# Kernel optimization log

Hardware: AMD Instinct MI355X
Metric: run time of the kernel (lower is better)

The kernel has to match this reference:

```python
import jax, jax.numpy as jnp
import numpy as np

VOCAB = 21
EPS = 1e-5


def rmsnorm(x, w):
    return x * jax.lax.rsqrt(jnp.mean(x * x, axis=-1, keepdims=True) + EPS) * w


def mamba_layer(h, in_w, conv_w, conv_b, xp_w, dtp_w, dtp_b, A_log, Dp, out_w):
    # h: (B, L, D)
    Bsz, L, _ = h.shape
    di, dc = conv_w.shape
    n = A_log.shape[-1]
    r = dtp_w.shape[-1]
    xz = jnp.einsum('bld,ed->ble', h, in_w)          # (B, L, 2*di)
    xi, z = jnp.split(xz, 2, axis=-1)
    # causal depthwise conv of width dc
    xp = jnp.pad(xi, ((0, 0), (dc - 1, 0), (0, 0)))
    xc = conv_b + sum(xp[:, k:k + L, :] * conv_w[:, k] for k in range(dc))
    xc = jax.nn.silu(xc)                              # (B, L, di)
    dbc = jnp.einsum('bld,ed->ble', xc, xp_w)         # (B, L, r+2n)
    dt, Bm, Cm = dbc[..., :r], dbc[..., r:r + n], dbc[..., r + n:]
    dt = jax.nn.softplus(jnp.einsum('blr,dr->bld', dt, dtp_w) + dtp_b)  # (B, L, di)
    A = -jnp.exp(A_log)                               # (di, n)

    def step(hst, inp):
        x_t, dt_t, B_t, C_t = inp                     # (B,di),(B,di),(B,n),(B,n)
        dA = jnp.exp(dt_t[..., None] * A)             # (B, di, n)
        hst = dA * hst + (dt_t * x_t)[..., None] * B_t[:, None, :]
        y_t = jnp.einsum('bdn,bn->bd', hst, C_t)
        return hst, y_t

    h0 = jnp.zeros((Bsz, di, n), dtype=h.dtype)
    xs = (xc.swapaxes(0, 1), dt.swapaxes(0, 1), Bm.swapaxes(0, 1), Cm.swapaxes(0, 1))
    _, ys = jax.lax.scan(step, h0, xs)
    y = ys.swapaxes(0, 1) + xc * Dp                   # skip term D*x
    y = y * jax.nn.silu(z)                            # gate
    return jnp.einsum('bld,ed->ble', y, out_w)


def setup_inputs() -> dict:
    key = jax.random.key(0)
    B, L, D = 4, 1024, 512
    n_layers, n, dc, expand = 2, 16, 3, 2
    di = expand * D
    r = (D + 15) // 16  # dt_rank = ceil(d_model/16) = 32
    ks = jax.random.split(key, 12)
    f32 = jnp.float32
    inp = {}
    inp['x'] = jax.random.randint(ks[0], (B, L), 0, VOCAB)
    inp['emb'] = 0.02 * jax.random.normal(ks[1], (VOCAB, D), f32)
    inp['norm_w'] = jnp.ones((n_layers, D), f32)
    inp['in_proj_w'] = (D ** -0.5) * jax.random.normal(ks[2], (n_layers, 2 * di, D), f32)
    inp['conv_w'] = (dc ** -0.5) * jax.random.normal(ks[3], (n_layers, di, dc), f32)
    inp['conv_b'] = jnp.zeros((n_layers, di), f32)
    inp['x_proj_w'] = (di ** -0.5) * jax.random.normal(ks[4], (n_layers, r + 2 * n, di), f32)
    inp['dt_proj_w'] = (r ** -0.5) * jax.random.normal(ks[5], (n_layers, di, r), f32)
    inp['dt_proj_b'] = jax.random.uniform(ks[6], (n_layers, di), f32, minval=-4.0, maxval=-1.0)
    inp['A_log'] = jnp.log(jnp.broadcast_to(jnp.arange(1, n + 1, dtype=f32), (n_layers, di, n)))
    inp['D_param'] = jnp.ones((n_layers, di), f32)
    inp['out_proj_w'] = (di ** -0.5) * jax.random.normal(ks[7], (n_layers, D, di), f32)
    inp['fc_w'] = (D ** -0.5) * jax.random.normal(ks[8], (2, D), f32)
    inp['fc_b'] = jnp.zeros((2,), f32)
    return inp


def reference(x, emb, norm_w, in_proj_w, conv_w, conv_b, x_proj_w, dt_proj_w,
              dt_proj_b, A_log, D_param, out_proj_w, fc_w, fc_b):
    h = emb[x].astype(jnp.float32)                    # (B, L, D)
    n_layers = norm_w.shape[0]
    for l in range(n_layers):
        h = rmsnorm(
            mamba_layer(h, in_proj_w[l], conv_w[l], conv_b[l], x_proj_w[l],
                        dt_proj_w[l], dt_proj_b[l], A_log[l], D_param[l],
                        out_proj_w[l]),
            norm_w[l])
    pooled = jnp.mean(h, axis=1)                      # global_pool=True
    out = jnp.tanh(pooled)                            # dropout is identity at eval
    return out @ fc_w.T + fc_b                        # (B, 2)
```

## Files before the change

kernel.cpp:

```cpp
#include <hip/hip_runtime.h>
#include <math.h>

constexpr int Bsz = 4, Lseq = 1024, Dmodel = 512, NLAYERS = 2;
constexpr int DI = 1024, NST = 16, RNK = 32;
constexpr int BLQ = Bsz * Lseq;
constexpr int NCH = 32, CLEN = 32;

typedef __attribute__((ext_vector_type(8))) short short8v;
typedef __attribute__((ext_vector_type(8))) unsigned short ushort8v;
typedef __attribute__((ext_vector_type(4))) float f32x4;
typedef unsigned short ushort;

__device__ inline ushort bf16_rne(float v) {
  unsigned u = __float_as_uint(v);
  u += 0x7FFFu + ((u >> 16) & 1u);
  return (ushort)(u >> 16);
}
__device__ inline float bf2f(ushort u) {
  return __uint_as_float(((unsigned)u) << 16);
}
__device__ inline size_t frag_off(int row, int k, int KT) {
  int kt = k >> 6, kk = (k >> 5) & 1, k8 = (k >> 3) & 3;
  int lanei = (row & 15) | (k8 << 4), msub = (row >> 4) & 7, rt = row >> 7;
  return ((((size_t)(rt * KT + kt) * 2 + kk) * 8 + msub) * 64 + lanei) * 8;
}

__global__ __launch_bounds__(256) void embed_kernel(const int* __restrict__ x,
    const float* __restrict__ emb, ushort* __restrict__ Af) {
  int i = blockIdx.x * 256 + threadIdx.x;
  int row = i >> 6, k = (i & 63) * 8;
  int tok = x[row];
  const float* src = &emb[(size_t)tok * Dmodel + k];
  float4 v0 = *reinterpret_cast<const float4*>(src);
  float4 v1 = *reinterpret_cast<const float4*>(src + 4);
  float xs[8] = {v0.x, v0.y, v0.z, v0.w, v1.x, v1.y, v1.z, v1.w};
  ushort hv[8];
#pragma unroll
  for (int e = 0; e < 8; ++e) hv[e] = bf16_rne(xs[e]);
  *reinterpret_cast<ushort8v*>(&Af[frag_off(row, k, 8)]) =
      *reinterpret_cast<ushort8v*>(hv);
}

__global__ __launch_bounds__(256) void cvtw_kernel(
    const float* __restrict__ in_w, const float* __restrict__ xp_w,
    const float* __restrict__ out_w,
    ushort* __restrict__ WIh, ushort* __restrict__ WIl,
    ushort* __restrict__ XPh, ushort* __restrict__ XPl,
    ushort* __restrict__ WOh, ushort* __restrict__ WOl)
{
  int blk = blockIdx.x;
  const float* src; ushort *dh, *dl; int KT; int row, k;
  if (blk < 1024) {
    int u = blk * 256 + threadIdx.x;
    int l = u >> 17, rem = u & 131071;
    row = rem >> 6; k = (rem & 63) * 8; KT = 8;
    src = in_w + (size_t)l * 2048 * 512 + (size_t)row * 512 + k;
    size_t base = (size_t)l * 2048 * 512;
    dh = WIh + base; dl = WIl + base;
  } else if (blk < 1088) {
    int u = (blk - 1024) * 256 + threadIdx.x;
    int l = u >> 13, rem = u & 8191;
    row = rem >> 7; k = (rem & 127) * 8; KT = 16;
    src = xp_w + (size_t)l * 64 * 1024 + (size_t)row * 1024 + k;
    size_t base = (size_t)l * 131072;
    dh = XPh + base; dl = XPl + base;
  } else {
    int u = (blk - 1088) * 256 + threadIdx.x;
    int l = u >> 16, rem = u & 65535;
    row = rem >> 7; k = (rem & 127) * 8; KT = 16;
    src = out_w + (size_t)l * 512 * 1024 + (size_t)row * 1024 + k;
    size_t base = (size_t)l * 512 * 1024;
    dh = WOh + base; dl = WOl + base;
  }
  float4 v0 = *reinterpret_cast<const float4*>(src);
  float4 v1 = *reinterpret_cast<const float4*>(src + 4);
  float xs[8] = {v0.x, v0.y, v0.z, v0.w, v1.x, v1.y, v1.z, v1.w};
  ushort hs[8], ls[8];
#pragma unroll
  for (int j = 0; j < 8; ++j) {
    unsigned u = __float_as_uint(xs[j]);
    float hf = __uint_as_float(u & 0xFFFF0000u);
    float r = xs[j] - hf;
    hs[j] = (ushort)(u >> 16);
    ls[j] = (ushort)(__float_as_uint(r) >> 16);
  }
  size_t d = frag_off(row, k, KT);
  *reinterpret_cast<ushort8v*>(&dh[d]) = *reinterpret_cast<ushort8v*>(hs);
  *reinterpret_cast<ushort8v*>(&dl[d]) = *reinterpret_cast<ushort8v*>(ls);
}

template<int OB>
__global__ __launch_bounds__(256) void gemm_mfma(
    const ushort* __restrict__ Ah,
    const ushort* __restrict__ Bh, const ushort* __restrict__ Bl,
    void* __restrict__ Cv, int N, int K)
{
  const int KT = K >> 6;
  constexpr int ASZ = 2 * 8 * 64 * 8;
  __shared__ ushort lds[3 * ASZ];
  const int tid = threadIdx.x;
  const int lane = tid & 63, wid = tid >> 6;
  const int wm = wid >> 1, wn = wid & 1;
  const int bm0 = blockIdx.y * 128, bn0 = blockIdx.x * 128;
  const size_t abase = (size_t)blockIdx.y * KT * ASZ;
  const size_t bbase = (size_t)blockIdx.x * KT * ASZ;
  const ushort* gsrc = (wid == 0) ? Ah : (wid == 1) ? Bh : Bl;
  const size_t gb = (wid == 0) ? abase : bbase;
  f32x4 acc[4][4];
#pragma unroll
  for (int i = 0; i < 4; ++i)
#pragma unroll
    for (int j = 0; j < 4; ++j) acc[i][j] = (f32x4){0.f, 0.f, 0.f, 0.f};
  const int msel = wm * 4, nsel = wn * 4;
  for (int kt = 0; kt < KT; ++kt) {
    if (wid < 3) {
      const ushort* sbase = gsrc + gb + (size_t)kt * ASZ + lane * 8;
#pragma unroll
      for (int i = 0; i < 16; ++i)
        __builtin_amdgcn_global_load_lds(
            (const __attribute__((address_space(1))) void*)(sbase + i * 512),
            (__attribute__((address_space(3))) void*)(lds + wid * ASZ + i * 512),
            16, 0, 0);
    }
    __syncthreads();
#pragma unroll
    for (int kk = 0; kk < 2; ++kk) {
      short8v a_h[4], b_h[4], b_l[4];
#pragma unroll
      for (int i = 0; i < 4; ++i) {
        int ai = ((kk * 8 + msel + i) * 64 + lane) * 8;
        int bi = ((kk * 8 + nsel + i) * 64 + lane) * 8;
        a_h[i] = *reinterpret_cast<const short8v*>(&lds[0 * ASZ + ai]);
        b_h[i] = *reinterpret_cast<const short8v*>(&lds[1 * ASZ + bi]);
        b_l[i] = *reinterpret_cast<const short8v*>(&lds[2 * ASZ + bi]);
      }
#pragma unroll
      for (int ms = 0; ms < 4; ++ms)
#pragma unroll
        for (int ns = 0; ns < 4; ++ns) {
          acc[ms][ns] = __builtin_amdgcn_mfma_f32_16x16x32_bf16(a_h[ms], b_h[ns], acc[ms][ns], 0, 0, 0);
          acc[ms][ns] = __builtin_amdgcn_mfma_f32_16x16x32_bf16(a_h[ms], b_l[ns], acc[ms][ns], 0, 0, 0);
        }
    }
    __syncthreads();
  }
  const int cr = lane >> 4, cc = lane & 15;
#pragma unroll
  for (int ms = 0; ms < 4; ++ms) {
    int row0 = bm0 + (msel + ms) * 16 + cr * 4;
#pragma unroll
    for (int ns = 0; ns < 4; ++ns) {
      int col = bn0 + (nsel + ns) * 16 + cc;
#pragma unroll
      for (int r = 0; r < 4; ++r) {
        if (OB) ((ushort*)Cv)[(size_t)(row0 + r) * N + col] = bf16_rne(acc[ms][ns][r]);
        else    ((float*)Cv)[(size_t)(row0 + r) * N + col] = acc[ms][ns][r];
      }
    }
  }
}

__global__ __launch_bounds__(256) void gemm_xp_mfma(
    const ushort* __restrict__ Ah,
    const ushort* __restrict__ Bh, const ushort* __restrict__ Bl,
    float* __restrict__ P)
{
  constexpr int ASZ = 2 * 8 * 64 * 8;
  __shared__ ushort lds[3 * ASZ];
  const int tid = threadIdx.x;
  const int lane = tid & 63, wid = tid >> 6;
  const int wm = wid >> 1, wn = wid & 1;
  const int bm0 = blockIdx.y * 128;
  const size_t abase = (size_t)blockIdx.y * 16 * ASZ;
  const ushort* gsrc = (wid == 0) ? Ah : (wid == 1) ? Bh : Bl;
  const size_t gb = (wid == 0) ? abase : 0;
  f32x4 acc[4][2];
#pragma unroll
  for (int i = 0; i < 4; ++i) { acc[i][0] = (f32x4){0,0,0,0}; acc[i][1] = (f32x4){0,0,0,0}; }
  const int msel = wm * 4, nsel = wn * 2;
  const int kt0 = blockIdx.z * 8;
  for (int kt = kt0; kt < kt0 + 8; ++kt) {
    if (wid < 3) {
      const ushort* sbase = gsrc + gb + (size_t)kt * ASZ + lane * 8;
#pragma unroll
      for (int i = 0; i < 16; ++i)
        __builtin_amdgcn_global_load_lds(
            (const __attribute__((address_space(1))) void*)(sbase + i * 512),
            (__attribute__((address_space(3))) void*)(lds + wid * ASZ + i * 512),
            16, 0, 0);
    }
    __syncthreads();
#pragma unroll
    for (int kk = 0; kk < 2; ++kk) {
      short8v a_h[4], b_h[2], b_l[2];
#pragma unroll
      for (int i = 0; i < 4; ++i) {
        int ai = ((kk * 8 + msel + i) * 64 + lane) * 8;
        a_h[i] = *reinterpret_cast<const short8v*>(&lds[0 * ASZ + ai]);
      }
#pragma unroll
      for (int i = 0; i < 2; ++i) {
        int bi = ((kk * 8 + nsel + i) * 64 + lane) * 8;
        b_h[i] = *reinterpret_cast<const short8v*>(&lds[1 * ASZ + bi]);
        b_l[i] = *reinterpret_cast<const short8v*>(&lds[2 * ASZ + bi]);
      }
#pragma unroll
      for (int ms = 0; ms < 4; ++ms)
#pragma unroll
        for (int ns = 0; ns < 2; ++ns) {
          acc[ms][ns] = __builtin_amdgcn_mfma_f32_16x16x32_bf16(a_h[ms], b_h[ns], acc[ms][ns], 0, 0, 0);
          acc[ms][ns] = __builtin_amdgcn_mfma_f32_16x16x32_bf16(a_h[ms], b_l[ns], acc[ms][ns], 0, 0, 0);
        }
    }
    __syncthreads();
  }
  float* Pz = P + (size_t)blockIdx.z * BLQ * 64;
  const int cr = lane >> 4, cc = lane & 15;
#pragma unroll
  for (int ms = 0; ms < 4; ++ms) {
    int row0 = bm0 + (msel + ms) * 16 + cr * 4;
#pragma unroll
    for (int ns = 0; ns < 2; ++ns) {
      int col = (nsel + ns) * 16 + cc;
#pragma unroll
      for (int r = 0; r < 4; ++r)
        Pz[(size_t)(row0 + r) * 64 + col] = acc[ms][ns][r];
    }
  }
}

__global__ __launch_bounds__(256) void conv_silu_kernel(
    const ushort* __restrict__ XZb, const float* __restrict__ cw,
    const float* __restrict__ cb, float* __restrict__ XC,
    ushort* __restrict__ XCf)
{
  int idx = blockIdx.x * 256 + threadIdx.x;
  int d8 = idx & 127;
  int bl = idx >> 7;
  int l = bl & (Lseq - 1);
  size_t base = (size_t)bl * (2 * DI) + d8 * 8;
  ushort8v cur = *reinterpret_cast<const ushort8v*>(&XZb[base]);
  ushort8v p1v = {}, p2v = {};
  if (l >= 1) p1v = *reinterpret_cast<const ushort8v*>(&XZb[base - 2 * DI]);
  if (l >= 2) p2v = *reinterpret_cast<const ushort8v*>(&XZb[base - 4 * DI]);
  float wv[24], bv[8];
#pragma unroll
  for (int q = 0; q < 6; ++q)
    *reinterpret_cast<float4*>(&wv[q * 4]) =
        *reinterpret_cast<const float4*>(&cw[d8 * 24 + q * 4]);
  *reinterpret_cast<float4*>(&bv[0]) = *reinterpret_cast<const float4*>(&cb[d8 * 8]);
  *reinterpret_cast<float4*>(&bv[4]) = *reinterpret_cast<const float4*>(&cb[d8 * 8 + 4]);
  float os[8];
  ushort hv[8];
#pragma unroll
  for (int e = 0; e < 8; ++e) {
    float acc = bv[e];
    acc = fmaf(bf2f(p2v[e]), wv[e * 3 + 0], acc);
    acc = fmaf(bf2f(p1v[e]), wv[e * 3 + 1], acc);
    acc = fmaf(bf2f(cur[e]), wv[e * 3 + 2], acc);
    float s = acc / (1.f + __expf(-acc));
    os[e] = s;
    hv[e] = bf16_rne(s);
  }
  float* op = &XC[(size_t)bl * DI + d8 * 8];
  *reinterpret_cast<float4*>(op) = *reinterpret_cast<float4*>(&os[0]);
  *reinterpret_cast<float4*>(op + 4) = *reinterpret_cast<float4*>(&os[4]);
  *reinterpret_cast<ushort8v*>(&XCf[frag_off(bl, d8 * 8, 16)]) =
      *reinterpret_cast<ushort8v*>(hv);
}

__global__ __launch_bounds__(256) void xpost_kernel(
    const float* __restrict__ P, const float* __restrict__ dtw,
    const float* __restrict__ dtb, float* __restrict__ DTb,
    float* __restrict__ BCc)
{
  const int tid = threadIdx.x;
  const size_t SL = (size_t)BLQ * 64;
  if (blockIdx.y == 16) {
    int i0 = blockIdx.x * 4096 + tid;
#pragma unroll
    for (int i = 0; i < 16; ++i) {
      int idx = i0 + i * 256;
      int bt = idx >> 5, n = idx & 31;
      size_t g = (size_t)bt * 64 + 32 + n;
      BCc[idx] = P[g] + P[SL + g];
    }
    return;
  }
  const int dg = blockIdx.y, bm0 = blockIdx.x * 128;
  __shared__ float db[128][33];
  __shared__ float wt[64][33];
#pragma unroll
  for (int i = 0; i < 16; ++i) {
    int e = tid + i * 256;
    int r = e >> 5, c = e & 31;
    size_t g = (size_t)(bm0 + r) * 64 + c;
    db[r][c] = P[g] + P[SL + g];
  }
#pragma unroll
  for (int i = 0; i < 8; ++i) {
    int e = tid + i * 256;
    int r = e >> 5, c = e & 31;
    wt[r][c] = dtw[(size_t)(dg * 64 + r) * 32 + c];
  }
  __syncthreads();
  const int d_loc = tid & 63, wv = tid >> 6;
  const float bias = dtb[dg * 64 + d_loc];
#pragma unroll 4
  for (int i = 0; i < 32; ++i) {
    int r = wv + i * 4;
    float dot = 0.f;
#pragma unroll
    for (int c = 0; c < 32; ++c) dot = fmaf(db[r][c], wt[d_loc][c], dot);
    float v = dot + bias;
    DTb[(size_t)(bm0 + r) * DI + dg * 64 + d_loc] =
        (v > 15.f) ? v : log1pf(__expf(v));
  }
}

__global__ __launch_bounds__(256) void scan_p1_kernel(
    const float* __restrict__ DTb, const float* __restrict__ XC,
    const float* __restrict__ BCc, const float* __restrict__ Alog,
    float* __restrict__ HEND, float* __restrict__ DSUM)
{
  const int d = blockIdx.x * 256 + threadIdx.x;
  const int c = blockIdx.y, b = blockIdx.z;
  const int t0 = b * Lseq + c * CLEN;
  __shared__ float Bs[CLEN][16];
#pragma unroll
  for (int i = 0; i < 2; ++i) {
    int e = threadIdx.x + i * 256;
    Bs[e >> 4][e & 15] = BCc[(size_t)(t0 + (e >> 4)) * 32 + (e & 15)];
  }
  float An[16];
#pragma unroll
  for (int j = 0; j < 4; ++j) {
    float4 a = *reinterpret_cast<const float4*>(&Alog[d * 16 + j * 4]);
    An[j * 4 + 0] = -__expf(a.x); An[j * 4 + 1] = -__expf(a.y);
    An[j * 4 + 2] = -__expf(a.z); An[j * 4 + 3] = -__expf(a.w);
  }
  __syncthreads();
  float h[16] = {};
  float S = 0.f;
  for (int t = 0; t < CLEN; ++t) {
    size_t g = (size_t)(t0 + t) * DI + d;
    float dt = DTb[g], xc = XC[g];
    S += dt;
    float dtxc = dt * xc;
#pragma unroll
    for (int n = 0; n < 16; ++n)
      h[n] = fmaf(__expf(An[n] * dt), h[n], dtxc * Bs[t][n]);
  }
  size_t hb = ((size_t)(b * NCH + c) * DI + d) * 16;
#pragma unroll
  for (int j = 0; j < 4; ++j)
    *reinterpret_cast<float4*>(&HEND[hb + j * 4]) =
        *reinterpret_cast<float4*>(&h[j * 4]);
  DSUM[(size_t)(b * NCH + c) * DI + d] = S;
}

__global__ __launch_bounds__(256) void scan_p2_kernel(
    float* __restrict__ HEND, const float* __restrict__ DSUM,
    const float* __restrict__ Alog)
{
  int id = blockIdx.x * 256 + threadIdx.x;
  int n = id & 15, d = (id >> 4) & (DI - 1), b = id >> 14;
  float An = -__expf(Alog[d * 16 + n]);
  float hg = 0.f;
  for (int c = 0; c < NCH; ++c) {
    size_t hi = ((size_t)(b * NCH + c) * DI + d) * 16 + n;
    float hl = HEND[hi];
    float Dc = DSUM[(size_t)(b * NCH + c) * DI + d];
    HEND[hi] = hg;
    hg = fmaf(__expf(An * Dc), hg, hl);
  }
}

__global__ __launch_bounds__(256) void scan_p3_kernel(
    const float* __restrict__ XC, const float* __restrict__ DTb,
    const float* __restrict__ BCc, const ushort* __restrict__ XZb,
    const float* __restrict__ HEND, const float* __restrict__ Alog,
    const float* __restrict__ Dp, ushort* __restrict__ Af)
{
  const int tid = threadIdx.x;
  const int dg = blockIdx.x, c = blockIdx.y, b = blockIdx.z;
  const int d = dg * 256 + tid;
  const int t0 = b * Lseq + c * CLEN;
  __shared__ float BC[CLEN][32];
  __shared__ float ys[CLEN][264];
#pragma unroll
  for (int i = 0; i < 4; ++i) {
    int e = tid + i * 256;
    BC[e >> 5][e & 31] = BCc[(size_t)(t0 + (e >> 5)) * 32 + (e & 31)];
  }
  float An[16], h[16];
  size_t hb = ((size_t)(b * NCH + c) * DI + d) * 16;
#pragma unroll
  for (int j = 0; j < 4; ++j) {
    float4 a = *reinterpret_cast<const float4*>(&Alog[d * 16 + j * 4]);
    An[j * 4 + 0] = -__expf(a.x); An[j * 4 + 1] = -__expf(a.y);
    An[j * 4 + 2] = -__expf(a.z); An[j * 4 + 3] = -__expf(a.w);
    *reinterpret_cast<float4*>(&h[j * 4]) =
        *reinterpret_cast<const float4*>(&HEND[hb + j * 4]);
  }
  float Dpv = Dp[d];
  __syncthreads();
  for (int t = 0; t < CLEN; ++t) {
    size_t g = (size_t)(t0 + t) * DI + d;
    float dt = DTb[g], xc = XC[g];
    float z = bf2f(XZb[(size_t)(t0 + t) * (2 * DI) + DI + d]);
    float dtxc = dt * xc;
    float y = 0.f;
#pragma unroll
    for (int n = 0; n < 16; ++n) {
      h[n] = fmaf(__expf(An[n] * dt), h[n], dtxc * BC[t][n]);
      y = fmaf(h[n], BC[t][16 + n], y);
    }
    float sil = z / (1.f + __expf(-z));
    ys[t][tid] = (y + xc * Dpv) * sil;
  }
  __syncthreads();
#pragma unroll
  for (int i = 0; i < 4; ++i) {
    int u = tid + i * 256;
    int tt = u >> 5, j8 = u & 31;
    int row = t0 + tt;
    int kg = dg * 256 + j8 * 8;
    ushort hv[8];
#pragma unroll
    for (int e = 0; e < 8; ++e) hv[e] = bf16_rne(ys[tt][j8 * 8 + e]);
    *reinterpret_cast<ushort8v*>(&Af[frag_off(row, kg, 16)]) =
        *reinterpret_cast<ushort8v*>(hv);
  }
}

__global__ __launch_bounds__(256) void rmsnorm_kernel(const float* __restrict__ X,
    const float* __restrict__ W, float* __restrict__ O, ushort* __restrict__ Af) {
  int row = blockIdx.x * 4 + (threadIdx.x >> 6);
  int lane = threadIdx.x & 63;
  int k = lane * 8;
  const float* xp = X + (size_t)row * Dmodel + k;
  float4 v0 = *reinterpret_cast<const float4*>(xp);
  float4 v1 = *reinterpret_cast<const float4*>(xp + 4);
  float vs[8] = {v0.x, v0.y, v0.z, v0.w, v1.x, v1.y, v1.z, v1.w};
  float ss = 0.f;
#pragma unroll
  for (int e = 0; e < 8; ++e) ss = fmaf(vs[e], vs[e], ss);
#pragma unroll
  for (int o = 32; o >= 1; o >>= 1) ss += __shfl_xor(ss, o);
  float sc = rsqrtf(ss * (1.f / Dmodel) + 1e-5f);
  const float* wp = W + k;
  float4 w0 = *reinterpret_cast<const float4*>(wp);
  float4 w1 = *reinterpret_cast<const float4*>(wp + 4);
  float wsv[8] = {w0.x, w0.y, w0.z, w0.w, w1.x, w1.y, w1.z, w1.w};
  float os[8];
  ushort hv[8];
#pragma unroll
  for (int e = 0; e < 8; ++e) {
    os[e] = vs[e] * sc * wsv[e];
    hv[e] = bf16_rne(os[e]);
  }
  float* op = O + (size_t)row * Dmodel + k;
  *reinterpret_cast<float4*>(op) = *reinterpret_cast<float4*>(&os[0]);
  *reinterpret_cast<float4*>(op + 4) = *reinterpret_cast<float4*>(&os[4]);
  *reinterpret_cast<ushort8v*>(&Af[frag_off(row, k, 8)]) =
      *reinterpret_cast<ushort8v*>(hv);
}

__global__ __launch_bounds__(256) void pool_part_kernel(const float* __restrict__ H,
    float* __restrict__ part) {
  int b = blockIdx.x, dg = blockIdx.y, tc = blockIdx.z;
  int tid = threadIdx.x;
  int d = dg * 128 + (tid & 127);
  int ph = tid >> 7;
  const float* base = H + ((size_t)(b * Lseq + tc * 128 + ph * 64)) * Dmodel + d;
  float s = 0.f;
#pragma unroll 8
  for (int t = 0; t < 64; ++t) s += base[(size_t)t * Dmodel];
  __shared__ float red[256];
  red[tid] = s; __syncthreads();
  if (ph == 0)
    part[(size_t)(b * 8 + tc) * Dmodel + d] = red[tid] + red[tid + 128];
}

__global__ __launch_bounds__(256) void pool_head_kernel(
    const float* __restrict__ part, const float* __restrict__ fcw,
    const float* __restrict__ fcb, float* __restrict__ out) {
  int b = blockIdx.x >> 1, j = blockIdx.x & 1;
  int tid = threadIdx.x;
  float s = 0.f;
  for (int d = tid; d < Dmodel; d += 256) {
    float p = 0.f;
#pragma unroll
    for (int tc = 0; tc < 8; ++tc) p += part[(size_t)(b * 8 + tc) * Dmodel + d];
    s += tanhf(p * (1.f / Lseq)) * fcw[j * Dmodel + d];
  }
#pragma unroll
  for (int o = 32; o >= 1; o >>= 1) s += __shfl_xor(s, o);
  __shared__ float w[4];
  if ((tid & 63) == 0) w[tid >> 6] = s;
  __syncthreads();
  if (tid == 0) out[b * 2 + j] = w[0] + w[1] + w[2] + w[3] + fcb[j];
}

extern "C" void kernel_launch(void* const* d_in, const int* in_sizes, int n_in,
                              void* d_out, int out_size, void* d_ws, size_t ws_size,
                              hipStream_t stream) {
  const int*   x      = (const int*)d_in[0];
  const float* emb    = (const float*)d_in[1];
  const float* norm_w = (const float*)d_in[2];
  const float* in_w   = (const float*)d_in[3];
  const float* conv_w = (const float*)d_in[4];
  const float* conv_b = (const float*)d_in[5];
  const float* xp_w   = (const float*)d_in[6];
  const float* dtp_w  = (const float*)d_in[7];
  const float* dtp_b  = (const float*)d_in[8];
  const float* A_log  = (const float*)d_in[9];
  const float* Dp     = (const float*)d_in[10];
  const float* out_w  = (const float*)d_in[11];
  const float* fc_w   = (const float*)d_in[12];
  const float* fc_b   = (const float*)d_in[13];
  float* out = (float*)d_out;

  char* p = (char*)d_ws;
  auto alloc = [&](size_t bytes) { char* r = p; p += (bytes + 255) & ~255ull; return r; };
  ushort* XZb  = (ushort*)alloc((size_t)BLQ * 2 * DI * 2);
  float*  XC   = (float*) alloc((size_t)BLQ * DI * 4);
  ushort* XCf  = (ushort*)alloc((size_t)BLQ * DI * 2);
  float*  DTb  = (float*) alloc((size_t)BLQ * DI * 4);
  float*  BCc  = (float*) alloc((size_t)BLQ * 32 * 4);
  float*  DBCP = (float*) alloc((size_t)2 * BLQ * 64 * 4);
  float*  HEND = (float*) alloc((size_t)Bsz * NCH * DI * 16 * 4);
  float*  DSUM = (float*) alloc((size_t)Bsz * NCH * DI * 4);
  float*  H    = (float*) alloc((size_t)BLQ * Dmodel * 4);
  float*  H2   = (float*) alloc((size_t)BLQ * Dmodel * 4);
  float*  PPART= (float*) alloc((size_t)Bsz * 8 * Dmodel * 4);
  ushort* AhI  = (ushort*)alloc((size_t)BLQ * Dmodel * 2);
  ushort* AhO  = (ushort*)alloc((size_t)BLQ * DI * 2);
  ushort* WIh  = (ushort*)alloc((size_t)2 * 2048 * 512 * 2);
  ushort* WIl  = (ushort*)alloc((size_t)2 * 2048 * 512 * 2);
  ushort* XPh  = (ushort*)alloc((size_t)2 * 131072 * 2);
  ushort* XPl  = (ushort*)alloc((size_t)2 * 131072 * 2);
  ushort* WOh  = (ushort*)alloc((size_t)2 * 512 * 1024 * 2);
  ushort* WOl  = (ushort*)alloc((size_t)2 * 512 * 1024 * 2);

  embed_kernel<<<BLQ * Dmodel / 8 / 256, 256, 0, stream>>>(x, emb, AhI);
  cvtw_kernel<<<1600, 256, 0, stream>>>(in_w, xp_w, out_w,
                                        WIh, WIl, XPh, XPl, WOh, WOl);

  for (int l = 0; l < NLAYERS; ++l) {
    const float* cw  = conv_w + (size_t)l * DI * 3;
    const float* cb  = conv_b + (size_t)l * DI;
    const float* dtw = dtp_w + (size_t)l * DI * RNK;
    const float* dtb = dtp_b + (size_t)l * DI;
    const float* Al  = A_log + (size_t)l * DI * NST;
    const float* dpl = Dp    + (size_t)l * DI;
    const float* nw  = norm_w + (size_t)l * Dmodel;
    const ushort* wih = WIh + (size_t)l * 2048 * 512;
    const ushort* wil = WIl + (size_t)l * 2048 * 512;
    const ushort* xph = XPh + (size_t)l * 131072;
    const ushort* xpl = XPl + (size_t)l * 131072;
    const ushort* woh = WOh + (size_t)l * 512 * 1024;
    const ushort* wol = WOl + (size_t)l * 512 * 1024;

    gemm_mfma<1><<<dim3(16, 32), 256, 0, stream>>>(AhI, wih, wil, XZb, 2 * DI, Dmodel);

    conv_silu_kernel<<<BLQ * DI / 8 / 256, 256, 0, stream>>>(XZb, cw, cb, XC, XCf);

    gemm_xp_mfma<<<dim3(1, 32, 2), 256, 0, stream>>>(XCf, xph, xpl, DBCP);

    xpost_kernel<<<dim3(32, 17), 256, 0, stream>>>(DBCP, dtw, dtb, DTb, BCc);

    scan_p1_kernel<<<dim3(DI / 256, NCH, Bsz), 256, 0, stream>>>(
        DTb, XC, BCc, Al, HEND, DSUM);
    scan_p2_kernel<<<Bsz * DI * NST / 256, 256, 0, stream>>>(HEND, DSUM, Al);
    scan_p3_kernel<<<dim3(DI / 256, NCH, Bsz), 256, 0, stream>>>(
        XC, DTb, BCc, XZb, HEND, Al, dpl, AhO);

    gemm_mfma<0><<<dim3(4, 32), 256, 0, stream>>>(AhO, woh, wol, H2, Dmodel, DI);

    rmsnorm_kernel<<<BLQ / 4, 256, 0, stream>>>(H2, nw, H, AhI);
  }

  pool_part_kernel<<<dim3(Bsz, Dmodel / 128, 8), 256, 0, stream>>>(H, PPART);
  pool_head_kernel<<<2 * Bsz, 256, 0, stream>>>(PPART, fc_w, fc_b, out);
}
```

Measured before the change: 311.6 us.

## Fuse conv+SiLU, x_proj GEMM and dt_proj softplus into one kernel

Replaces three kernels (conv_silu, split-K x_proj GEMM, and dt post-processing) with a single kernel. Each block handles 16 rows: it computes the causal conv and SiLU into LDS, runs the x_proj MFMA over K, then computes dt_proj with MFMA using dt_proj weights pre-split into bf16 hi/lo fragments. This removes the XCf and split-K partial buffers and two launches. In exchange each block covers only 16 rows with one MFMA tile per wave, so there is less parallelism and reuse per block, and the x_proj weights are re-read by every block.

After: 314.6 us. About the same (+0.9%).

```diff
diff --git a/kernel.cpp b/kernel.cpp
--- a/kernel.cpp
+++ b/kernel.cpp
@@ -24,6 +24,9 @@
   int lanei = (row & 15) | (k8 << 4), msub = (row >> 4) & 7, rt = row >> 7;
   return ((((size_t)(rt * KT + kt) * 2 + kk) * 8 + msub) * 64 + lanei) * 8;
 }
+#define GLDS(gp, lp) __builtin_amdgcn_global_load_lds( \
+    (const __attribute__((address_space(1))) void*)(gp), \
+    (__attribute__((address_space(3))) void*)(lp), 16, 0, 0)
 
 __global__ __launch_bounds__(256) void embed_kernel(const int* __restrict__ x,
     const float* __restrict__ emb, ushort* __restrict__ Af) {
@@ -43,34 +46,43 @@
 
 __global__ __launch_bounds__(256) void cvtw_kernel(
     const float* __restrict__ in_w, const float* __restrict__ xp_w,
-    const float* __restrict__ out_w,
+    const float* __restrict__ out_w, const float* __restrict__ dtp_w,
     ushort* __restrict__ WIh, ushort* __restrict__ WIl,
     ushort* __restrict__ XPh, ushort* __restrict__ XPl,
-    ushort* __restrict__ WOh, ushort* __restrict__ WOl)
+    ushort* __restrict__ WOh, ushort* __restrict__ WOl,
+    ushort* __restrict__ DTWh, ushort* __restrict__ DTWl)
 {
   int blk = blockIdx.x;
-  const float* src; ushort *dh, *dl; int KT; int row, k;
+  const float* src; ushort *dh, *dl; size_t doff;
   if (blk < 1024) {
     int u = blk * 256 + threadIdx.x;
     int l = u >> 17, rem = u & 131071;
-    row = rem >> 6; k = (rem & 63) * 8; KT = 8;
+    int row = rem >> 6, k = (rem & 63) * 8;
     src = in_w + (size_t)l * 2048 * 512 + (size_t)row * 512 + k;
     size_t base = (size_t)l * 2048 * 512;
-    dh = WIh + base; dl = WIl + base;
+    dh = WIh + base; dl = WIl + base; doff = frag_off(row, k, 8);
   } else if (blk < 1088) {
     int u = (blk - 1024) * 256 + threadIdx.x;
     int l = u >> 13, rem = u & 8191;
-    row = rem >> 7; k = (rem & 127) * 8; KT = 16;
+    int row = rem >> 7, k = (rem & 127) * 8;
     src = xp_w + (size_t)l * 64 * 1024 + (size_t)row * 1024 + k;
     size_t base = (size_t)l * 131072;
-    dh = XPh + base; dl = XPl + base;
-  } else {
+    dh = XPh + base; dl = XPl + base; doff = frag_off(row, k, 16);
+  } else if (blk < 1600) {
     int u = (blk - 1088) * 256 + threadIdx.x;
     int l = u >> 16, rem = u & 65535;
-    row = rem >> 7; k = (rem & 127) * 8; KT = 16;
+    int row = rem >> 7, k = (rem & 127) * 8;
     src = out_w + (size_t)l * 512 * 1024 + (size_t)row * 1024 + k;
     size_t base = (size_t)l * 512 * 1024;
-    dh = WOh + base; dl = WOl + base;
+    dh = WOh + base; dl = WOl + base; doff = frag_off(row, k, 16);
+  } else {
+    int u = (blk - 1600) * 256 + threadIdx.x;
+    int l = u >> 12, rem = u & 4095;
+    int n = rem >> 2, k8 = rem & 3, k = k8 * 8;
+    src = dtp_w + (size_t)l * 1024 * 32 + (size_t)n * 32 + k;
+    size_t base = (size_t)l * 32768;
+    dh = DTWh + base; dl = DTWl + base;
+    doff = (size_t)((n >> 4) * 64 + ((n & 15) | (k8 << 4))) * 8;
   }
   float4 v0 = *reinterpret_cast<const float4*>(src);
   float4 v1 = *reinterpret_cast<const float4*>(src + 4);
@@ -84,9 +96,8 @@
     hs[j] = (ushort)(u >> 16);
     ls[j] = (ushort)(__float_as_uint(r) >> 16);
   }
-  size_t d = frag_off(row, k, KT);
-  *reinterpret_cast<ushort8v*>(&dh[d]) = *reinterpret_cast<ushort8v*>(hs);
-  *reinterpret_cast<ushort8v*>(&dl[d]) = *reinterpret_cast<ushort8v*>(ls);
+  *reinterpret_cast<ushort8v*>(&dh[doff]) = *reinterpret_cast<ushort8v*>(hs);
+  *reinterpret_cast<ushort8v*>(&dl[doff]) = *reinterpret_cast<ushort8v*>(ls);
 }
 
 template<int OB>
@@ -117,10 +128,7 @@
       const ushort* sbase = gsrc + gb + (size_t)kt * ASZ + lane * 8;
 #pragma unroll
       for (int i = 0; i < 16; ++i)
-        __builtin_amdgcn_global_load_lds(
-            (const __attribute__((address_space(1))) void*)(sbase + i * 512),
-            (__attribute__((address_space(3))) void*)(lds + wid * ASZ + i * 512),
-            16, 0, 0);
+        GLDS(sbase + i * 512, lds + wid * ASZ + i * 512);
     }
     __syncthreads();
 #pragma unroll
@@ -160,161 +168,122 @@
   }
 }
 
-__global__ __launch_bounds__(256) void gemm_xp_mfma(
-    const ushort* __restrict__ Ah,
-    const ushort* __restrict__ Bh, const ushort* __restrict__ Bl,
-    float* __restrict__ P)
+__global__ __launch_bounds__(256) void convxp_kernel(
+    const ushort* __restrict__ XZb, const float* __restrict__ cw,
+    const float* __restrict__ cb,
+    const ushort* __restrict__ XPh, const ushort* __restrict__ XPl,
+    const ushort* __restrict__ DTWh, const ushort* __restrict__ DTWl,
+    const float* __restrict__ dtb,
+    float* __restrict__ XC, float* __restrict__ DTb, float* __restrict__ BCc)
 {
-  constexpr int ASZ = 2 * 8 * 64 * 8;
-  __shared__ ushort lds[3 * ASZ];
-  const int tid = threadIdx.x;
-  const int lane = tid & 63, wid = tid >> 6;
-  const int wm = wid >> 1, wn = wid & 1;
-  const int bm0 = blockIdx.y * 128;
-  const size_t abase = (size_t)blockIdx.y * 16 * ASZ;
-  const ushort* gsrc = (wid == 0) ? Ah : (wid == 1) ? Bh : Bl;
-  const size_t gb = (wid == 0) ? abase : 0;
-  f32x4 acc[4][2];
-#pragma unroll
-  for (int i = 0; i < 4; ++i) { acc[i][0] = (f32x4){0,0,0,0}; acc[i][1] = (f32x4){0,0,0,0}; }
-  const int msel = wm * 4, nsel = wn * 2;
-  const int kt0 = blockIdx.z * 8;
-  for (int kt = kt0; kt < kt0 + 8; ++kt) {
-    if (wid < 3) {
-      const ushort* sbase = gsrc + gb + (size_t)kt * ASZ + lane * 8;
-#pragma unroll
-      for (int i = 0; i < 16; ++i)
-        __builtin_amdgcn_global_load_lds(
-            (const __attribute__((address_space(1))) void*)(sbase + i * 512),
-            (__attribute__((address_space(3))) void*)(lds + wid * ASZ + i * 512),
-            16, 0, 0);
+  constexpr int XZOFF = 0;
+  constexpr int AOFF  = 1312;
+  constexpr int BHOFF = 2336;
+  constexpr int BLOFF = 6432;
+  __shared__ ushort smu[10528];
+  const int tid = threadIdx.x, lane = tid & 63, wid = tid >> 6;
+  const int cr = lane >> 4, cc = lane & 15;
+  const int bm0 = blockIdx.x * 16;
+  const int batchbase = bm0 & ~(Lseq - 1);
+  f32x4 acc = (f32x4){0.f, 0.f, 0.f, 0.f};
+
+  for (int kt = 0; kt < 16; ++kt) {
+    const int kcol0 = kt * 64;
+    if (wid < 2) {
+#pragma unroll
+      for (int i = 0; i < 2; ++i) {
+        int u = tid + i * 128;
+        if (u < 144) {
+          int r = u >> 3, c8 = u & 7;
+          int grow = bm0 - 2 + r;
+          ushort8v v = {};
+          if (grow >= batchbase)
+            v = *reinterpret_cast<const ushort8v*>(
+                &XZb[(size_t)grow * 2048 + kcol0 + c8 * 8]);
+          *reinterpret_cast<ushort8v*>(&smu[XZOFF + r * 72 + c8 * 8]) = v;
+        }
+      }
+    } else {
+      const ushort* src = ((wid == 2) ? XPh : XPl) + (size_t)kt * 8192 + lane * 8;
+      int dst0 = (wid == 2) ? BHOFF : BLOFF;
+#pragma unroll
+      for (int i = 0; i < 8; ++i) {
+        int sidx = (i >> 2) * 8 + (i & 3);
+        int didx = i;
+        GLDS(src + sidx * 512, smu + dst0 + didx * 512);
+      }
     }
     __syncthreads();
+    if (tid < 128) {
+      int row = tid >> 3, c8 = tid & 7;
+      int d0 = kcol0 + c8 * 8;
+      ushort8v cur = *reinterpret_cast<ushort8v*>(&smu[XZOFF + (row + 2) * 72 + c8 * 8]);
+      ushort8v pm1 = *reinterpret_cast<ushort8v*>(&smu[XZOFF + (row + 1) * 72 + c8 * 8]);
+      ushort8v pm2 = *reinterpret_cast<ushort8v*>(&smu[XZOFF + (row + 0) * 72 + c8 * 8]);
+      float wv[24], bv[8];
+#pragma unroll
+      for (int q = 0; q < 6; ++q)
+        *reinterpret_cast<float4*>(&wv[q * 4]) =
+            *reinterpret_cast<const float4*>(&cw[d0 * 3 + q * 4]);
+      *reinterpret_cast<float4*>(&bv[0]) = *reinterpret_cast<const float4*>(&cb[d0]);
+      *reinterpret_cast<float4*>(&bv[4]) = *reinterpret_cast<const float4*>(&cb[d0 + 4]);
+      float os[8]; ushort hv[8];
+#pragma unroll
+      for (int e = 0; e < 8; ++e) {
+        float a = bv[e];
+        a = fmaf(bf2f(pm2[e]), wv[e * 3 + 0], a);
+        a = fmaf(bf2f(pm1[e]), wv[e * 3 + 1], a);
+        a = fmaf(bf2f(cur[e]), wv[e * 3 + 2], a);
+        float s = a / (1.f + __expf(-a));
+        os[e] = s; hv[e] = bf16_rne(s);
+      }
+      float* op = &XC[(size_t)(bm0 + row) * DI + d0];
+      *reinterpret_cast<float4*>(op) = *reinterpret_cast<float4*>(&os[0]);
+      *reinterpret_cast<float4*>(op + 4) = *reinterpret_cast<float4*>(&os[4]);
+      int kk = c8 >> 2, k8 = c8 & 3;
+      int lanei = row | (k8 << 4);
+      *reinterpret_cast<ushort8v*>(&smu[AOFF + (kk * 64 + lanei) * 8]) =
+          *reinterpret_cast<ushort8v*>(hv);
+    }
+    __syncthreads();
 #pragma unroll
     for (int kk = 0; kk < 2; ++kk) {
-      short8v a_h[4], b_h[2], b_l[2];
-#pragma unroll
-      for (int i = 0; i < 4; ++i) {
-        int ai = ((kk * 8 + msel + i) * 64 + lane) * 8;
-        a_h[i] = *reinterpret_cast<const short8v*>(&lds[0 * ASZ + ai]);
-      }
-#pragma unroll
-      for (int i = 0; i < 2; ++i) {
-        int bi = ((kk * 8 + nsel + i) * 64 + lane) * 8;
-        b_h[i] = *reinterpret_cast<const short8v*>(&lds[1 * ASZ + bi]);
-        b_l[i] = *reinterpret_cast<const short8v*>(&lds[2 * ASZ + bi]);
-      }
-#pragma unroll
-      for (int ms = 0; ms < 4; ++ms)
-#pragma unroll
-        for (int ns = 0; ns < 2; ++ns) {
-          acc[ms][ns] = __builtin_amdgcn_mfma_f32_16x16x32_bf16(a_h[ms], b_h[ns], acc[ms][ns], 0, 0, 0);
-          acc[ms][ns] = __builtin_amdgcn_mfma_f32_16x16x32_bf16(a_h[ms], b_l[ns], acc[ms][ns], 0, 0, 0);
-        }
+      short8v a = *reinterpret_cast<const short8v*>(&smu[AOFF + (kk * 64 + lane) * 8]);
+      short8v bh = *reinterpret_cast<const short8v*>(&smu[BHOFF + ((kk * 4 + wid) * 64 + lane) * 8]);
+      short8v bl = *reinterpret_cast<const short8v*>(&smu[BLOFF + ((kk * 4 + wid) * 64 + lane) * 8]);
+      acc = __builtin_amdgcn_mfma_f32_16x16x32_bf16(a, bh, acc, 0, 0, 0);
+      acc = __builtin_amdgcn_mfma_f32_16x16x32_bf16(a, bl, acc, 0, 0, 0);
     }
     __syncthreads();
   }
-  float* Pz = P + (size_t)blockIdx.z * BLQ * 64;
-  const int cr = lane >> 4, cc = lane & 15;
-#pragma unroll
-  for (int ms = 0; ms < 4; ++ms) {
-    int row0 = bm0 + (msel + ms) * 16 + cr * 4;
-#pragma unroll
-    for (int ns = 0; ns < 2; ++ns) {
-      int col = (nsel + ns) * 16 + cc;
-#pragma unroll
-      for (int r = 0; r < 4; ++r)
-        Pz[(size_t)(row0 + r) * 64 + col] = acc[ms][ns][r];
-    }
-  }
-}
-
-__global__ __launch_bounds__(256) void conv_silu_kernel(
-    const ushort* __restrict__ XZb, const float* __restrict__ cw,
-    const float* __restrict__ cb, float* __restrict__ XC,
-    ushort* __restrict__ XCf)
-{
-  int idx = blockIdx.x * 256 + threadIdx.x;
-  int d8 = idx & 127;
-  int bl = idx >> 7;
-  int l = bl & (Lseq - 1);
-  size_t base = (size_t)bl * (2 * DI) + d8 * 8;
-  ushort8v cur = *reinterpret_cast<const ushort8v*>(&XZb[base]);
-  ushort8v p1v = {}, p2v = {};
-  if (l >= 1) p1v = *reinterpret_cast<const ushort8v*>(&XZb[base - 2 * DI]);
-  if (l >= 2) p2v = *reinterpret_cast<const ushort8v*>(&XZb[base - 4 * DI]);
-  float wv[24], bv[8];
-#pragma unroll
-  for (int q = 0; q < 6; ++q)
-    *reinterpret_cast<float4*>(&wv[q * 4]) =
-        *reinterpret_cast<const float4*>(&cw[d8 * 24 + q * 4]);
-  *reinterpret_cast<float4*>(&bv[0]) = *reinterpret_cast<const float4*>(&cb[d8 * 8]);
-  *reinterpret_cast<float4*>(&bv[4]) = *reinterpret_cast<const float4*>(&cb[d8 * 8 + 4]);
-  float os[8];
-  ushort hv[8];
-#pragma unroll
-  for (int e = 0; e < 8; ++e) {
-    float acc = bv[e];
-    acc = fmaf(bf2f(p2v[e]), wv[e * 3 + 0], acc);
-    acc = fmaf(bf2f(p1v[e]), wv[e * 3 + 1], acc);
-    acc = fmaf(bf2f(cur[e]), wv[e * 3 + 2], acc);
-    float s = acc / (1.f + __expf(-acc));
-    os[e] = s;
-    hv[e] = bf16_rne(s);
-  }
-  float* op = &XC[(size_t)bl * DI + d8 * 8];
-  *reinterpret_cast<float4*>(op) = *reinterpret_cast<float4*>(&os[0]);
-  *reinterpret_cast<float4*>(op + 4) = *reinterpret_cast<float4*>(&os[4]);
-  *reinterpret_cast<ushort8v*>(&XCf[frag_off(bl, d8 * 8, 16)]) =
-      *reinterpret_cast<ushort8v*>(hv);
-}
-
-__global__ __launch_bounds__(256) void xpost_kernel(
-    const float* __restrict__ P, const float* __restrict__ dtw,
-    const float* __restrict__ dtb, float* __restrict__ DTb,
-    float* __restrict__ BCc)
-{
-  const int tid = threadIdx.x;
-  const size_t SL = (size_t)BLQ * 64;
-  if (blockIdx.y == 16) {
-    int i0 = blockIdx.x * 4096 + tid;
-#pragma unroll
-    for (int i = 0; i < 16; ++i) {
-      int idx = i0 + i * 256;
-      int bt = idx >> 5, n = idx & 31;
-      size_t g = (size_t)bt * 64 + 32 + n;
-      BCc[idx] = P[g] + P[SL + g];
-    }
-    return;
-  }
-  const int dg = blockIdx.y, bm0 = blockIdx.x * 128;
-  __shared__ float db[128][33];
-  __shared__ float wt[64][33];
-#pragma unroll
+  if (wid >= 2) {
+#pragma unroll
+    for (int r = 0; r < 4; ++r)
+      BCc[(size_t)(bm0 + cr * 4 + r) * 32 + (wid - 2) * 16 + cc] = acc[r];
+  } else {
+    int k = wid * 16 + cc, k8 = k >> 3;
+#pragma unroll
+    for (int r = 0; r < 4; ++r)
+      smu[(((cr * 4 + r) | (k8 << 4)) * 8) + (k & 7)] = bf16_rne(acc[r]);
+  }
+  __syncthreads();
+  short8v a_dt = *reinterpret_cast<const short8v*>(&smu[lane * 8]);
+#pragma unroll 4
   for (int i = 0; i < 16; ++i) {
-    int e = tid + i * 256;
-    int r = e >> 5, c = e & 31;
-    size_t g = (size_t)(bm0 + r) * 64 + c;
-    db[r][c] = P[g] + P[SL + g];
-  }
-#pragma unroll
-  for (int i = 0; i < 8; ++i) {
-    int e = tid + i * 256;
-    int r = e >> 5, c = e & 31;
-    wt[r][c] = dtw[(size_t)(dg * 64 + r) * 32 + c];
-  }
-  __syncthreads();
-  const int d_loc = tid & 63, wv = tid >> 6;
-  const float bias = dtb[dg * 64 + d_loc];
-#pragma unroll 4
-  for (int i = 0; i < 32; ++i) {
-    int r = wv + i * 4;
-    float dot = 0.f;
-#pragma unroll
-    for (int c = 0; c < 32; ++c) dot = fmaf(db[r][c], wt[d_loc][c], dot);
-    float v = dot + bias;
-    DTb[(size_t)(bm0 + r) * DI + dg * 64 + d_loc] =
-        (v > 15.f) ? v : log1pf(__expf(v));
+    int nt = wid * 16 + i;
+    short8v bh = *reinterpret_cast<const short8v*>(&DTWh[(size_t)(nt * 64 + lane) * 8]);
+    short8v bl = *reinterpret_cast<const short8v*>(&DTWl[(size_t)(nt * 64 + lane) * 8]);
+    f32x4 p = (f32x4){0.f, 0.f, 0.f, 0.f};
+    p = __builtin_amdgcn_mfma_f32_16x16x32_bf16(a_dt, bh, p, 0, 0, 0);
+    p = __builtin_amdgcn_mfma_f32_16x16x32_bf16(a_dt, bl, p, 0, 0, 0);
+    int n = nt * 16 + cc;
+    float bias = dtb[n];
+#pragma unroll
+    for (int r = 0; r < 4; ++r) {
+      float v = p[r] + bias;
+      float sp = (v > 15.f) ? v : log1pf(__expf(v));
+      DTb[(size_t)(bm0 + cr * 4 + r) * DI + n] = sp;
+    }
   }
 }
 
@@ -526,10 +495,8 @@
   auto alloc = [&](size_t bytes) { char* r = p; p += (bytes + 255) & ~255ull; return r; };
   ushort* XZb  = (ushort*)alloc((size_t)BLQ * 2 * DI * 2);
   float*  XC   = (float*) alloc((size_t)BLQ * DI * 4);
-  ushort* XCf  = (ushort*)alloc((size_t)BLQ * DI * 2);
   float*  DTb  = (float*) alloc((size_t)BLQ * DI * 4);
   float*  BCc  = (float*) alloc((size_t)BLQ * 32 * 4);
-  float*  DBCP = (float*) alloc((size_t)2 * BLQ * 64 * 4);
   float*  HEND = (float*) alloc((size_t)Bsz * NCH * DI * 16 * 4);
   float*  DSUM = (float*) alloc((size_t)Bsz * NCH * DI * 4);
   float*  H    = (float*) alloc((size_t)BLQ * Dmodel * 4);
@@ -543,15 +510,16 @@
   ushort* XPl  = (ushort*)alloc((size_t)2 * 131072 * 2);
   ushort* WOh  = (ushort*)alloc((size_t)2 * 512 * 1024 * 2);
   ushort* WOl  = (ushort*)alloc((size_t)2 * 512 * 1024 * 2);
+  ushort* DTWh = (ushort*)alloc((size_t)2 * 32768 * 2);
+  ushort* DTWl = (ushort*)alloc((size_t)2 * 32768 * 2);
 
   embed_kernel<<<BLQ * Dmodel / 8 / 256, 256, 0, stream>>>(x, emb, AhI);
-  cvtw_kernel<<<1600, 256, 0, stream>>>(in_w, xp_w, out_w,
-                                        WIh, WIl, XPh, XPl, WOh, WOl);
+  cvtw_kernel<<<1632, 256, 0, stream>>>(in_w, xp_w, out_w, dtp_w,
+      WIh, WIl, XPh, XPl, WOh, WOl, DTWh, DTWl);
 
   for (int l = 0; l < NLAYERS; ++l) {
     const float* cw  = conv_w + (size_t)l * DI * 3;
     const float* cb  = conv_b + (size_t)l * DI;
-    const float* dtw = dtp_w + (size_t)l * DI * RNK;
     const float* dtb = dtp_b + (size_t)l * DI;
     const float* Al  = A_log + (size_t)l * DI * NST;
     const float* dpl = Dp    + (size_t)l * DI;
@@ -562,14 +530,13 @@
     const ushort* xpl = XPl + (size_t)l * 131072;
     const ushort* woh = WOh + (size_t)l * 512 * 1024;
     const ushort* wol = WOl + (size_t)l * 512 * 1024;
+    const ushort* dwh = DTWh + (size_t)l * 32768;
+    const ushort* dwl = DTWl + (size_t)l * 32768;
 
     gemm_mfma<1><<<dim3(16, 32), 256, 0, stream>>>(AhI, wih, wil, XZb, 2 * DI, Dmodel);
 
-    conv_silu_kernel<<<BLQ * DI / 8 / 256, 256, 0, stream>>>(XZb, cw, cb, XC, XCf);
-
-    gemm_xp_mfma<<<dim3(1, 32, 2), 256, 0, stream>>>(XCf, xph, xpl, DBCP);
-
-    xpost_kernel<<<dim3(32, 17), 256, 0, stream>>>(DBCP, dtw, dtb, DTb, BCc);
+    convxp_kernel<<<BLQ / 16, 256, 0, stream>>>(XZb, cw, cb, xph, xpl,
+        dwh, dwl, dtb, XC, DTb, BCc);
 
     scan_p1_kernel<<<dim3(DI / 256, NCH, Bsz), 256, 0, stream>>>(
         DTb, XC, BCc, Al, HEND, DSUM);
```
